# Kernel tuning notes

Hardware: AMD Instinct MI355X
Metric: run time of the kernel (lower is better)

The kernel has to match this reference:

```python
import jax, jax.numpy as jnp
import numpy as np

NUM_HEADS = 16
MAX_LEN = 1024  # RelativePositionalEncoding default


def setup_inputs() -> dict:
    key = jax.random.key(0)
    ks = jax.random.split(key, 12)
    S, B, E = 1024, 4, 1024
    hd = E // NUM_HEADS
    table = 2 * MAX_LEN - 1  # 2047
    mu = 1.0 / np.sqrt(E)
    def lin_w(k):
        return jax.random.uniform(k, (E, E), jnp.float32, -mu, mu)
    def lin_b(k):
        return jax.random.uniform(k, (E,), jnp.float32, -mu, mu)
    return {
        "query": jax.random.normal(ks[0], (S, B, E), jnp.float32),
        "key": jax.random.normal(ks[1], (S, B, E), jnp.float32),
        "value": jax.random.normal(ks[2], (S, B, E), jnp.float32),
        "Wq": lin_w(ks[3]), "bq": lin_b(ks[4]),
        "Wk": lin_w(ks[5]), "bk": lin_b(ks[6]),
        "Wv": lin_w(ks[7]), "bv": lin_b(ks[8]),
        "Wo": lin_w(ks[9]), "bo": lin_b(ks[10]),
        "rel_pos_table": jax.random.normal(ks[11], (table, hd), jnp.float32),
    }


def reference(query, key, value, Wq, bq, Wk, bk, Wv, bv, Wo, bo, rel_pos_table):
    S, B, E = query.shape
    H = NUM_HEADS
    hd = E // H
    scale = hd ** -0.5
    # eval-mode NoisyLoRALinear == plain linear with mu params
    q = (query @ Wq.T + bq).reshape(S, B, H, hd).transpose(1, 2, 0, 3) * scale  # [B,H,S,hd]
    k = (key @ Wk.T + bk).reshape(S, B, H, hd).transpose(1, 2, 0, 3)
    v = (value @ Wv.T + bv).reshape(S, B, H, hd).transpose(1, 2, 0, 3)
    content = jnp.einsum('bhsd,bhtd->bhst', q, k)  # [B,H,S,S]
    # relative position embeddings: rel_pos_table[final_mat] -> [S,S,hd]
    L = rel_pos_table.shape[0]  # 2*max_len - 1
    half = L // 2
    r = jnp.arange(S)
    dist = r[None, :] - r[:, None]
    idx = jnp.clip(dist, -half + 1, half - 1) + half - 1
    rel_emb = rel_pos_table[idx]  # [S,S,hd]
    pos = jnp.einsum('bhsd,std->bhst', q, rel_emb)
    attn = jax.nn.softmax(content + pos, axis=-1)
    out = jnp.einsum('bhst,bhtd->bhsd', attn, v)  # [B,H,S,hd]
    out = out.transpose(0, 2, 1, 3).reshape(B, S, E)
    out = out @ Wo.T + bo  # [B,S,E]
    return out.transpose(1, 0, 2)  # [S,B,E]
```

## Files before the change

### kernel.cpp

```cpp
#include <hip/hip_runtime.h>
#include <math.h>

#define S_LEN 1024
#define B_SZ 4
#define E_DIM 1024
#define H_NUM 16
#define HD 64
#define IDX_MAX 2044
#define NEG_BIG (-3.0e38f)

typedef __attribute__((ext_vector_type(8))) short s16x8;
typedef __attribute__((ext_vector_type(4))) float f32x4;

__device__ __forceinline__ unsigned short f2bf(float f) {
  union { float f; unsigned int u; } v; v.f = f;
  return (unsigned short)((v.u + 0x7FFFu + ((v.u >> 16) & 1u)) >> 16);
}
__device__ __forceinline__ float bf2f(unsigned short h) {
  union { unsigned int u; float f; } v; v.u = ((unsigned int)h) << 16;
  return v.f;
}
__device__ __forceinline__ void gload16(const void* g, void* l) {
  __builtin_amdgcn_global_load_lds(
      (const __attribute__((address_space(1))) void*)g,
      (__attribute__((address_space(3))) void*)l, 16, 0, 0);
}
__device__ __forceinline__ int clampg(int g) {
  return g < 0 ? 0 : (g > IDX_MAX ? IDX_MAX : g);
}

template <int CTRL>
__device__ __forceinline__ float dppror(float x) {
  union { float f; int i; } a, b;
  a.f = x;
  b.i = __builtin_amdgcn_update_dpp(a.i, a.i, CTRL, 0xF, 0xF, false);
  return b.f;
}
__device__ __forceinline__ float rmax16(float x) {
  x = fmaxf(x, dppror<0x128>(x));
  x = fmaxf(x, dppror<0x124>(x));
  x = fmaxf(x, dppror<0x122>(x));
  x = fmaxf(x, dppror<0x121>(x));
  return x;
}
__device__ __forceinline__ float rsum16(float x) {
  x += dppror<0x128>(x);
  x += dppror<0x124>(x);
  x += dppror<0x122>(x);
  x += dppror<0x121>(x);
  return x;
}

__global__ __launch_bounds__(256) void conv_all(
    const float* __restrict__ q, const float* __restrict__ k,
    const float* __restrict__ v, const float* __restrict__ wq,
    const float* __restrict__ wk, const float* __restrict__ wv,
    const float* __restrict__ wo, const float* __restrict__ tb,
    unsigned short* __restrict__ oq, unsigned short* __restrict__ ok,
    unsigned short* __restrict__ ov, unsigned short* __restrict__ owq,
    unsigned short* __restrict__ owk, unsigned short* __restrict__ owv,
    unsigned short* __restrict__ owo, unsigned short* __restrict__ otb)
{
  const int b = blockIdx.x;
  const float* src; unsigned short* dst; int n, lb;
  if (b < 2048)      { src = q;  dst = oq;  n = 4194304; lb = b; }
  else if (b < 4096) { src = k;  dst = ok;  n = 4194304; lb = b - 2048; }
  else if (b < 6144) { src = v;  dst = ov;  n = 4194304; lb = b - 4096; }
  else if (b < 6656) { src = wq; dst = owq; n = 1048576; lb = b - 6144; }
  else if (b < 7168) { src = wk; dst = owk; n = 1048576; lb = b - 6656; }
  else if (b < 7680) { src = wv; dst = owv; n = 1048576; lb = b - 7168; }
  else if (b < 8192) { src = wo; dst = owo; n = 1048576; lb = b - 7680; }
  else               { src = tb; dst = otb; n = 131008;  lb = b - 8192; }
  const int i = (lb * 256 + threadIdx.x) << 3;
  if (i >= n) return;
  const float4 a = *(const float4*)(src + i);
  const float4 c = *(const float4*)(src + i + 4);
  union { unsigned short us[8]; uint4 v4; } u;
  u.us[0] = f2bf(a.x); u.us[1] = f2bf(a.y); u.us[2] = f2bf(a.z); u.us[3] = f2bf(a.w);
  u.us[4] = f2bf(c.x); u.us[5] = f2bf(c.y); u.us[6] = f2bf(c.z); u.us[7] = f2bf(c.w);
  *(uint4*)(dst + i) = u.v4;
}

__global__ __launch_bounds__(256, 3) void qkv_mfma(
    const unsigned short* __restrict__ X0, const unsigned short* __restrict__ X1,
    const unsigned short* __restrict__ X2,
    const unsigned short* __restrict__ W0, const unsigned short* __restrict__ W1,
    const unsigned short* __restrict__ W2,
    const float* __restrict__ bp0, const float* __restrict__ bp1,
    const float* __restrict__ bp2,
    unsigned short* __restrict__ O0, unsigned short* __restrict__ O1,
    unsigned short* __restrict__ O2)
{
  __shared__ unsigned short As[128 * 64];
  __shared__ unsigned short Bs[128 * 64];

  const int z = blockIdx.z;
  const unsigned short* X = z == 0 ? X0 : (z == 1 ? X1 : X2);
  const unsigned short* W = z == 0 ? W0 : (z == 1 ? W1 : W2);
  const float* bias = z == 0 ? bp0 : (z == 1 ? bp1 : bp2);
  unsigned short* O = z == 0 ? O0 : (z == 1 ? O1 : O2);
  const float scale = z == 0 ? 0.125f : 1.0f;

  const int tid = threadIdx.x;
  const int w = tid >> 6, l = tid & 63;
  const int l15 = l & 15, l4 = l >> 4;
  const int m0 = blockIdx.x << 7, n0 = blockIdx.y << 7;
  const int wr0 = (w >> 1) << 6, wc0 = (w & 1) << 6;

  f32x4 acc[4][4];
#pragma unroll
  for (int mt = 0; mt < 4; ++mt)
#pragma unroll
    for (int nt = 0; nt < 4; ++nt) acc[mt][nt] = (f32x4){0.f, 0.f, 0.f, 0.f};

  float bias4[4];
#pragma unroll
  for (int nt = 0; nt < 4; ++nt) bias4[nt] = bias[n0 + wc0 + (nt << 4) + l15];

  const int cbase = (w << 6) + l;

  for (int kt = 0; kt < 16; ++kt) {
    const int k0 = kt << 6;
    __syncthreads();
#pragma unroll
    for (int i = 0; i < 4; ++i) {
      const int c = cbase + (i << 8);
      const int r = c >> 3, kc = c & 7;
      char* ldsA = (char*)As + (((i << 2) + w) << 10);
      char* ldsB = (char*)Bs + (((i << 2) + w) << 10);
      gload16(X + (size_t)(m0 + r) * E_DIM + k0 + (kc << 3), ldsA);
      gload16(W + (size_t)(n0 + r) * E_DIM + k0 + (kc << 3), ldsB);
    }
    __syncthreads();
#pragma unroll
    for (int kh = 0; kh < 2; ++kh) {
      s16x8 af[4], bfr[4];
#pragma unroll
      for (int mt = 0; mt < 4; ++mt)
        af[mt] = *(const s16x8*)&As[(wr0 + (mt << 4) + l15) * 64 + (kh << 5) + (l4 << 3)];
#pragma unroll
      for (int nt = 0; nt < 4; ++nt)
        bfr[nt] = *(const s16x8*)&Bs[(wc0 + (nt << 4) + l15) * 64 + (kh << 5) + (l4 << 3)];
#pragma unroll
      for (int mt = 0; mt < 4; ++mt)
#pragma unroll
        for (int nt = 0; nt < 4; ++nt)
          acc[mt][nt] = __builtin_amdgcn_mfma_f32_16x16x32_bf16(
              af[mt], bfr[nt], acc[mt][nt], 0, 0, 0);
    }
  }

#pragma unroll
  for (int mt = 0; mt < 4; ++mt)
#pragma unroll
    for (int nt = 0; nt < 4; ++nt) {
      const int n = n0 + wc0 + (nt << 4) + l15;
      const int h = n >> 6, d = n & 63;
      const f32x4 c = acc[mt][nt];
#pragma unroll
      for (int r = 0; r < 4; ++r) {
        const int m = m0 + wr0 + (mt << 4) + (l4 << 2) + r;
        const int s = m >> 2, b = m & 3;
        O[((((size_t)b * H_NUM + h) * S_LEN) + s) * HD + d] =
            f2bf((c[r] + bias4[nt]) * scale);
      }
    }
}

__global__ __launch_bounds__(256) void outp_mfma(
    const unsigned short* __restrict__ Ah, const unsigned short* __restrict__ Al,
    const unsigned short* __restrict__ W, const float* __restrict__ bias,
    float* __restrict__ out)
{
  __shared__ unsigned short Ahs[128 * 64];
  __shared__ unsigned short Als[128 * 64];
  __shared__ unsigned short Bs[128 * 64];

  const int tid = threadIdx.x;
  const int w = tid >> 6, l = tid & 63;
  const int l15 = l & 15, l4 = l >> 4;
  const int m0 = blockIdx.x << 7, n0 = blockIdx.y << 7;
  const int wr0 = (w >> 1) << 6, wc0 = (w & 1) << 6;

  f32x4 acc[4][4];
#pragma unroll
  for (int mt = 0; mt < 4; ++mt)
#pragma unroll
    for (int nt = 0; nt < 4; ++nt) acc[mt][nt] = (f32x4){0.f, 0.f, 0.f, 0.f};

  float bias4[4];
#pragma unroll
  for (int nt = 0; nt < 4; ++nt) bias4[nt] = bias[n0 + wc0 + (nt << 4) + l15];

  const int cbase = (w << 6) + l;

  for (int kt = 0; kt < 16; ++kt) {
    const int k0 = kt << 6;
    __syncthreads();
#pragma unroll
    for (int i = 0; i < 4; ++i) {
      const int c = cbase + (i << 8);
      const int r = c >> 3, kc = c & 7;
      char* ldsAh = (char*)Ahs + (((i << 2) + w) << 10);
      char* ldsAl = (char*)Als + (((i << 2) + w) << 10);
      char* ldsB  = (char*)Bs  + (((i << 2) + w) << 10);
      gload16(Ah + (size_t)(m0 + r) * E_DIM + k0 + (kc << 3), ldsAh);
      gload16(Al + (size_t)(m0 + r) * E_DIM + k0 + (kc << 3), ldsAl);
      gload16(W  + (size_t)(n0 + r) * E_DIM + k0 + (kc << 3), ldsB);
    }
    __syncthreads();
#pragma unroll
    for (int kh = 0; kh < 2; ++kh) {
      s16x8 ah[4], al[4], bfr[4];
      const int ko = (kh << 5) + (l4 << 3);
#pragma unroll
      for (int mt = 0; mt < 4; ++mt) {
        ah[mt] = *(const s16x8*)&Ahs[(wr0 + (mt << 4) + l15) * 64 + ko];
        al[mt] = *(const s16x8*)&Als[(wr0 + (mt << 4) + l15) * 64 + ko];
      }
#pragma unroll
      for (int nt = 0; nt < 4; ++nt)
        bfr[nt] = *(const s16x8*)&Bs[(wc0 + (nt << 4) + l15) * 64 + ko];
#pragma unroll
      for (int mt = 0; mt < 4; ++mt)
#pragma unroll
        for (int nt = 0; nt < 4; ++nt) {
          acc[mt][nt] = __builtin_amdgcn_mfma_f32_16x16x32_bf16(
              ah[mt], bfr[nt], acc[mt][nt], 0, 0, 0);
          acc[mt][nt] = __builtin_amdgcn_mfma_f32_16x16x32_bf16(
              al[mt], bfr[nt], acc[mt][nt], 0, 0, 0);
        }
    }
  }

#pragma unroll
  for (int mt = 0; mt < 4; ++mt)
#pragma unroll
    for (int nt = 0; nt < 4; ++nt) {
      const int n = n0 + wc0 + (nt << 4) + l15;
      const f32x4 c = acc[mt][nt];
#pragma unroll
      for (int r = 0; r < 4; ++r) {
        const int m = m0 + wr0 + (mt << 4) + (l4 << 2) + r;
        const int b = m >> 10, s = m & 1023;
        out[((size_t)s * B_SZ + b) * E_DIM + n] = c[r] + bias4[nt];
      }
    }
}

__global__ __launch_bounds__(256) void attn_mfma(
    const unsigned short* __restrict__ Qb, const unsigned short* __restrict__ Kb,
    const unsigned short* __restrict__ Vb, const unsigned short* __restrict__ Rb,
    unsigned short* __restrict__ AOh, unsigned short* __restrict__ AOl)
{
  __shared__ unsigned short Ks[64 * 64];
  __shared__ unsigned short Rs[64 * 64];
  __shared__ unsigned short Vt[64 * 64];
  __shared__ unsigned short Ps[64 * 64];
  __shared__ float band[64 * 132];

  const int tid = threadIdx.x;
  const int lane = tid & 63;
  const int w = tid >> 6;
  const int st = blockIdx.x & 15;
  const int bh = blockIdx.x >> 4;
  const int s0 = st << 6;
  const int bb = bh >> 4, hh = bh & 15;
  const size_t base = (size_t)bh * (S_LEN * HD);
  const int l15 = lane & 15, l4 = lane >> 4;
  const int rb_ = w << 4;

  const int sr = tid >> 3, scb = tid & 7;
  const int ksl = (scb ^ (sr & 7)) << 3;
  const int jp = tid >> 3, vc = tid & 7;
  const int jc = jp >> 2, jlow = (jp & 3) << 1;

  const int rbase = 959 - s0;

  s16x8 qf0, qf1;
  {
    const unsigned short* qp =
        Qb + base + (size_t)(s0 + rb_ + l15) * HD + (l4 << 3);
    qf0 = *(const s16x8*)(qp);
    qf1 = *(const s16x8*)(qp + 32);
  }

  f32x4 of[4];
  float mrow[4], lrow[4];
#pragma unroll
  for (int m = 0; m < 4; ++m) {
    of[m] = (f32x4){0.f, 0.f, 0.f, 0.f};
    mrow[m] = NEG_BIG; lrow[m] = 0.f;
  }

#define BAND_MFMA(H0)                                                          \
  {                                                                            \
    f32x4 bq[4];                                                               \
    _Pragma("unroll") for (int rt = 0; rt < 4; ++rt)                           \
        bq[rt] = (f32x4){0.f, 0.f, 0.f, 0.f};                                  \
    __builtin_amdgcn_s_setprio(1);                                             \
    _Pragma("unroll") for (int kk = 0; kk < 2; ++kk) {                         \
      const s16x8 qv = kk ? qf1 : qf0;                                         \
      const int cb = l4 + (kk << 2);                                           \
      _Pragma("unroll") for (int rt = 0; rt < 4; ++rt) {                       \
        const int r = (rt << 4) + l15;                                         \
        const s16x8 rf = *(const s16x8*)&Rs[(r << 6) + ((cb ^ (r & 7)) << 3)]; \
        bq[rt] = __builtin_amdgcn_mfma_f32_16x16x32_bf16(qv, rf, bq[rt], 0, 0, 0); \
      }                                                                        \
    }                                                                          \
    __builtin_amdgcn_s_setprio(0);                                             \
    _Pragma("unroll") for (int rt = 0; rt < 4; ++rt)                           \
      _Pragma("unroll") for (int m = 0; m < 4; ++m)                            \
        band[(rb_ + (l4 << 2) + m) * 132 + (H0) + (rt << 4) + l15] = bq[rt][m];\
  }

  s16x8 Kr0, Kr1, Vr0, Vr1, Rr0, Rr1;
  {
    s16x8 tA0, tA1, tB0, tB1;
    tA0 = *(const s16x8*)(Rb + (size_t)clampg(rbase + sr) * HD + (scb << 3));
    tA1 = *(const s16x8*)(Rb + (size_t)clampg(rbase + 32 + sr) * HD + (scb << 3));
    tB0 = *(const s16x8*)(Rb + (size_t)clampg(rbase + 64 + sr) * HD + (scb << 3));
    tB1 = *(const s16x8*)(Rb + (size_t)clampg(rbase + 96 + sr) * HD + (scb << 3));
    *(s16x8*)&Rs[(sr << 6) + ksl] = tA0;
    *(s16x8*)&Rs[((sr + 32) << 6) + ksl] = tA1;
    __syncthreads();
    BAND_MFMA(0);
    Kr0 = *(const s16x8*)(Kb + base + (size_t)sr * HD + (scb << 3));
    Kr1 = *(const s16x8*)(Kb + base + (size_t)(32 + sr) * HD + (scb << 3));
    Vr0 = *(const s16x8*)(Vb + base + (size_t)(jp << 1) * HD + (vc << 3));
    Vr1 = *(const s16x8*)(Vb + base + (size_t)((jp << 1) + 1) * HD + (vc << 3));
    Rr0 = *(const s16x8*)(Rb + (size_t)clampg(rbase + 128 + sr) * HD + (scb << 3));
    Rr1 = *(const s16x8*)(Rb + (size_t)clampg(rbase + 160 + sr) * HD + (scb << 3));
    __syncthreads();
    *(s16x8*)&Rs[(sr << 6) + ksl] = tB0;
    *(s16x8*)&Rs[((sr + 32) << 6) + ksl] = tB1;
    __syncthreads();
    BAND_MFMA(64);
  }

  for (int tt = 0; tt < 16; ++tt) {
    const int t0 = tt << 6;
    __syncthreads();

    *(s16x8*)&Ks[(sr << 6) + ksl] = Kr0;
    *(s16x8*)&Ks[((sr + 32) << 6) + ksl] = Kr1;
    *(s16x8*)&Rs[(sr << 6) + ksl] = Rr0;
    *(s16x8*)&Rs[((sr + 32) << 6) + ksl] = Rr1;
#pragma unroll
    for (int e = 0; e < 8; ++e) {
      const int d = (vc << 3) + e;
      const int slot = jc ^ e ^ vc;
      const unsigned int pack = (unsigned int)(unsigned short)Vr0[e] |
                                ((unsigned int)(unsigned short)Vr1[e] << 16);
      *(unsigned int*)&Vt[(d << 6) + (slot << 3) + jlow] = pack;
    }
    __syncthreads();

    if (tt < 15) {
      const int tn = t0 + 64;
      Kr0 = *(const s16x8*)(Kb + base + (size_t)(tn + sr) * HD + (scb << 3));
      Kr1 = *(const s16x8*)(Kb + base + (size_t)(tn + 32 + sr) * HD + (scb << 3));
      Vr0 = *(const s16x8*)(Vb + base + (size_t)(tn + (jp << 1)) * HD + (vc << 3));
      Vr1 = *(const s16x8*)(Vb + base + (size_t)(tn + (jp << 1) + 1) * HD + (vc << 3));
      const int gb = rbase + ((tt + 3) << 6) + sr;
      Rr0 = *(const s16x8*)(Rb + (size_t)clampg(gb) * HD + (scb << 3));
      Rr1 = *(const s16x8*)(Rb + (size_t)clampg(gb + 32) * HD + (scb << 3));
    }

    f32x4 cf[4];
#pragma unroll
    for (int jt = 0; jt < 4; ++jt) cf[jt] = (f32x4){0.f, 0.f, 0.f, 0.f};
    __builtin_amdgcn_s_setprio(1);
#pragma unroll
    for (int kk = 0; kk < 2; ++kk) {
      const s16x8 qv = kk ? qf1 : qf0;
      const int cb = l4 + (kk << 2);
#pragma unroll
      for (int jt = 0; jt < 4; ++jt) {
        const int r = (jt << 4) + l15;
        const s16x8 kf = *(const s16x8*)&Ks[(r << 6) + ((cb ^ (r & 7)) << 3)];
        cf[jt] = __builtin_amdgcn_mfma_f32_16x16x32_bf16(qv, kf, cf[jt], 0, 0, 0);
      }
    }
    __builtin_amdgcn_s_setprio(0);

#pragma unroll
    for (int m = 0; m < 4; ++m) {
      const int irow = rb_ + (l4 << 2) + m;
      const int bc = t0 + 63 - irow;
      const float* bp = &band[irow * 132];
      float sv[4];
#pragma unroll
      for (int jt = 0; jt < 4; ++jt)
        sv[jt] = cf[jt][m] + bp[(bc + (jt << 4) + l15) & 127];
      float mx = fmaxf(fmaxf(sv[0], sv[1]), fmaxf(sv[2], sv[3]));
      mx = rmax16(mx);
      const float mnew = fmaxf(mrow[m], mx);
      const float alpha = __expf(mrow[m] - mnew);
      float p[4], ls = 0.f;
#pragma unroll
      for (int jt = 0; jt < 4; ++jt) { p[jt] = __expf(sv[jt] - mnew); ls += p[jt]; }
      ls = rsum16(ls);
      lrow[m] = lrow[m] * alpha + ls;
      mrow[m] = mnew;
#pragma unroll
      for (int dt = 0; dt < 4; ++dt) of[dt][m] *= alpha;
#pragma unroll
      for (int jt = 0; jt < 4; ++jt) {
        const int col = (jt << 4) + l15;
        const int ch = col >> 3;
        Ps[(irow << 6) + ((ch ^ (irow & 7)) << 3) + (col & 7)] = f2bf(p[jt]);
      }
    }

    BAND_MFMA((tt & 1) << 6);

    __builtin_amdgcn_s_setprio(1);
#pragma unroll
    for (int kk = 0; kk < 2; ++kk) {
      const int cb = l4 + (kk << 2);
      const int pr = rb_ + l15;
      const s16x8 pf = *(const s16x8*)&Ps[(pr << 6) + ((cb ^ (pr & 7)) << 3)];
#pragma unroll
      for (int dt = 0; dt < 4; ++dt) {
        const int dr = (dt << 4) + l15;
        const int slot = cb ^ (dr & 7) ^ ((dt << 1) + (l15 >> 3));
        const s16x8 vf = *(const s16x8*)&Vt[(dr << 6) + (slot << 3)];
        of[dt] = __builtin_amdgcn_mfma_f32_16x16x32_bf16(pf, vf, of[dt], 0, 0, 0);
      }
    }
    __builtin_amdgcn_s_setprio(0);
  }

#pragma unroll
  for (int m = 0; m < 4; ++m) {
    const float inv = 1.f / lrow[m];
    const int srow = s0 + rb_ + (l4 << 2) + m;
    const size_t off0 = ((size_t)bb * S_LEN + srow) * E_DIM + (hh << 6) + l15;
#pragma unroll
    for (int dt = 0; dt < 4; ++dt) {
      const float x = of[dt][m] * inv;
      const unsigned short hi = f2bf(x);
      AOh[off0 + (dt << 4)] = hi;
      AOl[off0 + (dt << 4)] = f2bf(x - bf2f(hi));
    }
  }
#undef BAND_MFMA
}

extern "C" void kernel_launch(void* const* d_in, const int* in_sizes, int n_in,
                              void* d_out, int out_size, void* d_ws, size_t ws_size,
                              hipStream_t stream) {
  (void)in_sizes; (void)n_in; (void)out_size; (void)ws_size;
  const float* query = (const float*)d_in[0];
  const float* key   = (const float*)d_in[1];
  const float* value = (const float*)d_in[2];
  const float* Wq = (const float*)d_in[3];
  const float* bq = (const float*)d_in[4];
  const float* Wk = (const float*)d_in[5];
  const float* bk = (const float*)d_in[6];
  const float* Wv = (const float*)d_in[7];
  const float* bv = (const float*)d_in[8];
  const float* Wo = (const float*)d_in[9];
  const float* bo = (const float*)d_in[10];
  const float* tbl = (const float*)d_in[11];

  const size_t per = (size_t)B_SZ * H_NUM * S_LEN * HD;
  const size_t wsz = (size_t)E_DIM * E_DIM;
  unsigned short* p = (unsigned short*)d_ws;
  unsigned short* wsQb = p; p += per;
  unsigned short* wsKb = p; p += per;
  unsigned short* wsVb = p; p += per;
  unsigned short* wsRb = p; p += 131072;
  unsigned short* wsXq = p; p += per;
  unsigned short* wsXk = p; p += per;
  unsigned short* wsXv = p; p += per;
  unsigned short* wsWq = p; p += wsz;
  unsigned short* wsWk = p; p += wsz;
  unsigned short* wsWv = p; p += wsz;
  unsigned short* wsWo = p; p += wsz;
  unsigned short* wsAh = p; p += per;
  unsigned short* wsAl = p; p += per;
  float* out = (float*)d_out;

  dim3 blk(256);
  hipLaunchKernelGGL(conv_all, dim3(8256), blk, 0, stream,
                     query, key, value, Wq, Wk, Wv, Wo, tbl,
                     wsXq, wsXk, wsXv, wsWq, wsWk, wsWv, wsWo, wsRb);
  hipLaunchKernelGGL(qkv_mfma, dim3(32, 8, 3), blk, 0, stream,
                     wsXq, wsXk, wsXv, wsWq, wsWk, wsWv, bq, bk, bv,
                     wsQb, wsKb, wsVb);
  hipLaunchKernelGGL(attn_mfma, dim3(1024), blk, 0, stream,
                     wsQb, wsKb, wsVb, wsRb, wsAh, wsAl);
  hipLaunchKernelGGL(outp_mfma, dim3(32, 8), blk, 0, stream,
                     wsAh, wsAl, wsWo, bo, out);
}
```

Measured before the change: 163.2 us.

## Fuse fp32-to-bf16 activation conversion into QKV GEMM with register prefetch

The separate conversion pass over the query, key and value activations is removed. The QKV GEMM now loads fp32 activations straight into registers one k-tile ahead, converts them to bf16, and writes them into LDS, while the weights still come in through global_load_lds. This drops roughly 48MB of conversion traffic and one write-back, at the cost of extra register pressure and reading X in fp32 eight times across the N tiles. The attention kernel also reorders its block-to-(batch,head,tile) mapping for cache locality and changes the P-tile LDS swizzle to cut bank conflicts.

New measurement: 165.2 us. No clear change (+1.2%).

```diff
diff --git a/kernel.cpp b/kernel.cpp
--- a/kernel.cpp
+++ b/kernel.cpp
@@ -51,26 +51,21 @@
   return x;
 }
 
-__global__ __launch_bounds__(256) void conv_all(
-    const float* __restrict__ q, const float* __restrict__ k,
-    const float* __restrict__ v, const float* __restrict__ wq,
-    const float* __restrict__ wk, const float* __restrict__ wv,
-    const float* __restrict__ wo, const float* __restrict__ tb,
-    unsigned short* __restrict__ oq, unsigned short* __restrict__ ok,
-    unsigned short* __restrict__ ov, unsigned short* __restrict__ owq,
-    unsigned short* __restrict__ owk, unsigned short* __restrict__ owv,
-    unsigned short* __restrict__ owo, unsigned short* __restrict__ otb)
+__global__ __launch_bounds__(256) void conv_w(
+    const float* __restrict__ wq, const float* __restrict__ wk,
+    const float* __restrict__ wv, const float* __restrict__ wo,
+    const float* __restrict__ tb,
+    unsigned short* __restrict__ owq, unsigned short* __restrict__ owk,
+    unsigned short* __restrict__ owv, unsigned short* __restrict__ owo,
+    unsigned short* __restrict__ otb)
 {
   const int b = blockIdx.x;
   const float* src; unsigned short* dst; int n, lb;
-  if (b < 2048)      { src = q;  dst = oq;  n = 4194304; lb = b; }
-  else if (b < 4096) { src = k;  dst = ok;  n = 4194304; lb = b - 2048; }
-  else if (b < 6144) { src = v;  dst = ov;  n = 4194304; lb = b - 4096; }
-  else if (b < 6656) { src = wq; dst = owq; n = 1048576; lb = b - 6144; }
-  else if (b < 7168) { src = wk; dst = owk; n = 1048576; lb = b - 6656; }
-  else if (b < 7680) { src = wv; dst = owv; n = 1048576; lb = b - 7168; }
-  else if (b < 8192) { src = wo; dst = owo; n = 1048576; lb = b - 7680; }
-  else               { src = tb; dst = otb; n = 131008;  lb = b - 8192; }
+  if (b < 512)       { src = wq; dst = owq; n = 1048576; lb = b; }
+  else if (b < 1024) { src = wk; dst = owk; n = 1048576; lb = b - 512; }
+  else if (b < 1536) { src = wv; dst = owv; n = 1048576; lb = b - 1024; }
+  else if (b < 2048) { src = wo; dst = owo; n = 1048576; lb = b - 1536; }
+  else               { src = tb; dst = otb; n = 131008;  lb = b - 2048; }
   const int i = (lb * 256 + threadIdx.x) << 3;
   if (i >= n) return;
   const float4 a = *(const float4*)(src + i);
@@ -82,8 +77,8 @@
 }
 
 __global__ __launch_bounds__(256, 3) void qkv_mfma(
-    const unsigned short* __restrict__ X0, const unsigned short* __restrict__ X1,
-    const unsigned short* __restrict__ X2,
+    const float* __restrict__ X0, const float* __restrict__ X1,
+    const float* __restrict__ X2,
     const unsigned short* __restrict__ W0, const unsigned short* __restrict__ W1,
     const unsigned short* __restrict__ W2,
     const float* __restrict__ bp0, const float* __restrict__ bp1,
@@ -95,7 +90,7 @@
   __shared__ unsigned short Bs[128 * 64];
 
   const int z = blockIdx.z;
-  const unsigned short* X = z == 0 ? X0 : (z == 1 ? X1 : X2);
+  const float* X = z == 0 ? X0 : (z == 1 ? X1 : X2);
   const unsigned short* W = z == 0 ? W0 : (z == 1 ? W1 : W2);
   const float* bias = z == 0 ? bp0 : (z == 1 ? bp1 : bp2);
   unsigned short* O = z == 0 ? O0 : (z == 1 ? O1 : O2);
@@ -117,21 +112,41 @@
 #pragma unroll
   for (int nt = 0; nt < 4; ++nt) bias4[nt] = bias[n0 + wc0 + (nt << 4) + l15];
 
+  const int xr = tid >> 3, xc = (tid & 7) << 3;
+  const float* Xp = X + (size_t)(m0 + xr) * E_DIM + xc;
   const int cbase = (w << 6) + l;
+
+  float4 xa[4][2];
+#define LOADX(K0)                                                              \
+  _Pragma("unroll") for (int p4 = 0; p4 < 4; ++p4) {                           \
+    const float* s_ = Xp + (size_t)(p4 << 5) * E_DIM + (K0);                   \
+    xa[p4][0] = *(const float4*)(s_);                                          \
+    xa[p4][1] = *(const float4*)(s_ + 4);                                      \
+  }
+
+  LOADX(0);
 
   for (int kt = 0; kt < 16; ++kt) {
     const int k0 = kt << 6;
     __syncthreads();
+#pragma unroll
+    for (int p4 = 0; p4 < 4; ++p4) {
+      union { unsigned short us[8]; s16x8 v; } u;
+      u.us[0] = f2bf(xa[p4][0].x); u.us[1] = f2bf(xa[p4][0].y);
+      u.us[2] = f2bf(xa[p4][0].z); u.us[3] = f2bf(xa[p4][0].w);
+      u.us[4] = f2bf(xa[p4][1].x); u.us[5] = f2bf(xa[p4][1].y);
+      u.us[6] = f2bf(xa[p4][1].z); u.us[7] = f2bf(xa[p4][1].w);
+      *(s16x8*)&As[(xr + (p4 << 5)) * 64 + xc] = u.v;
+    }
 #pragma unroll
     for (int i = 0; i < 4; ++i) {
       const int c = cbase + (i << 8);
       const int r = c >> 3, kc = c & 7;
-      char* ldsA = (char*)As + (((i << 2) + w) << 10);
       char* ldsB = (char*)Bs + (((i << 2) + w) << 10);
-      gload16(X + (size_t)(m0 + r) * E_DIM + k0 + (kc << 3), ldsA);
       gload16(W + (size_t)(n0 + r) * E_DIM + k0 + (kc << 3), ldsB);
     }
     __syncthreads();
+    if (kt < 15) LOADX(k0 + 64);
 #pragma unroll
     for (int kh = 0; kh < 2; ++kh) {
       s16x8 af[4], bfr[4];
@@ -149,6 +164,7 @@
               af[mt], bfr[nt], acc[mt][nt], 0, 0, 0);
     }
   }
+#undef LOADX
 
 #pragma unroll
   for (int mt = 0; mt < 4; ++mt)
@@ -247,6 +263,8 @@
       }
     }
 }
+
+#define HSW(r) (((r) & 7) ^ ((((r) >> 3) & 1) * 3))
 
 __global__ __launch_bounds__(256) void attn_mfma(
     const unsigned short* __restrict__ Qb, const unsigned short* __restrict__ Kb,
@@ -262,8 +280,10 @@
   const int tid = threadIdx.x;
   const int lane = tid & 63;
   const int w = tid >> 6;
-  const int st = blockIdx.x & 15;
-  const int bh = blockIdx.x >> 4;
+  const int x = blockIdx.x;
+  const int idx = x >> 3;
+  const int bh = (x & 7) + ((idx & 7) << 3);
+  const int st = idx >> 3;
   const int s0 = st << 6;
   const int bb = bh >> 4, hh = bh & 15;
   const size_t base = (size_t)bh * (S_LEN * HD);
@@ -409,7 +429,7 @@
       for (int jt = 0; jt < 4; ++jt) {
         const int col = (jt << 4) + l15;
         const int ch = col >> 3;
-        Ps[(irow << 6) + ((ch ^ (irow & 7)) << 3) + (col & 7)] = f2bf(p[jt]);
+        Ps[(irow << 6) + ((ch ^ HSW(irow)) << 3) + (col & 7)] = f2bf(p[jt]);
       }
     }
 
@@ -420,7 +440,7 @@
     for (int kk = 0; kk < 2; ++kk) {
       const int cb = l4 + (kk << 2);
       const int pr = rb_ + l15;
-      const s16x8 pf = *(const s16x8*)&Ps[(pr << 6) + ((cb ^ (pr & 7)) << 3)];
+      const s16x8 pf = *(const s16x8*)&Ps[(pr << 6) + ((cb ^ HSW(pr)) << 3)];
 #pragma unroll
       for (int dt = 0; dt < 4; ++dt) {
         const int dr = (dt << 4) + l15;
@@ -439,14 +459,15 @@
     const size_t off0 = ((size_t)bb * S_LEN + srow) * E_DIM + (hh << 6) + l15;
 #pragma unroll
     for (int dt = 0; dt < 4; ++dt) {
-      const float x = of[dt][m] * inv;
-      const unsigned short hi = f2bf(x);
+      const float x2 = of[dt][m] * inv;
+      const unsigned short hi = f2bf(x2);
       AOh[off0 + (dt << 4)] = hi;
-      AOl[off0 + (dt << 4)] = f2bf(x - bf2f(hi));
+      AOl[off0 + (dt << 4)] = f2bf(x2 - bf2f(hi));
     }
   }
 #undef BAND_MFMA
 }
+#undef HSW
 
 extern "C" void kernel_launch(void* const* d_in, const int* in_sizes, int n_in,
                               void* d_out, int out_size, void* d_ws, size_t ws_size,
@@ -472,9 +493,6 @@
   unsigned short* wsKb = p; p += per;
   unsigned short* wsVb = p; p += per;
   unsigned short* wsRb = p; p += 131072;
-  unsigned short* wsXq = p; p += per;
-  unsigned short* wsXk = p; p += per;
-  unsigned short* wsXv = p; p += per;
   unsigned short* wsWq = p; p += wsz;
   unsigned short* wsWk = p; p += wsz;
   unsigned short* wsWv = p; p += wsz;
@@ -484,11 +502,10 @@
   float* out = (float*)d_out;
 
   dim3 blk(256);
-  hipLaunchKernelGGL(conv_all, dim3(8256), blk, 0, stream,
-                     query, key, value, Wq, Wk, Wv, Wo, tbl,
-                     wsXq, wsXk, wsXv, wsWq, wsWk, wsWv, wsWo, wsRb);
+  hipLaunchKernelGGL(conv_w, dim3(2112), blk, 0, stream,
+                     Wq, Wk, Wv, Wo, tbl, wsWq, wsWk, wsWv, wsWo, wsRb);
   hipLaunchKernelGGL(qkv_mfma, dim3(32, 8, 3), blk, 0, stream,
-                     wsXq, wsXk, wsXv, wsWq, wsWk, wsWv, bq, bk, bv,
+                     query, key, value, wsWq, wsWk, wsWv, bq, bk, bv,
                      wsQb, wsKb, wsVb);
   hipLaunchKernelGGL(attn_mfma, dim3(1024), blk, 0, stream,
                      wsQb, wsKb, wsVb, wsRb, wsAh, wsAl);
```
